# Performance work log

Measured on AMD Instinct MI355X. Metric: run time of the kernel, lower is better.

The kernel has to match this reference:

```python
import jax, jax.numpy as jnp
import numpy as np

P = 3  # spline degree in both u and v (init_kwargs degrees=[3,3])


def _knot_vector(n_cp, p):
    # clamped uniform knot vector, length n_cp+p+1 (matches calculate_knot_vectors)
    kv = np.concatenate([np.zeros(p), np.linspace(0.0, 1.0, n_cp - p + 1), np.ones(p)])
    return jnp.asarray(kv.astype(np.float32))


def _basis_and_deriv(u, spans, knots, p):
    # Cox-de Boor basis functions and 1st derivatives (NURBS Book A2.3), vectorized
    # u, spans: [S,F,E]; knots: 1D. Returns (N, dN) each [S,F,E,p+1].
    left = [None] * (p + 1)
    right = [None] * (p + 1)
    ndu = [[None] * (p + 1) for _ in range(p + 1)]
    ndu[0][0] = jnp.ones_like(u)
    for j in range(1, p + 1):
        left[j] = u - knots[spans - j + 1]
        right[j] = knots[spans + j] - u
        saved = jnp.zeros_like(u)
        for r in range(j):
            ndu[j][r] = right[r + 1] + left[j - r]  # knot differences
            tmp = ndu[r][j - 1] / ndu[j][r]
            ndu[r][j] = saved + right[r + 1] * tmp
            saved = left[j - r] * tmp
        ndu[j][j] = saved
    n = 1  # nth_derivative = 1
    ders = [[jnp.zeros_like(u) for _ in range(p + 1)] for _ in range(n + 1)]
    for j in range(p + 1):
        ders[0][j] = ndu[j][p]
    for r in range(p + 1):
        a = [[jnp.zeros_like(u) for _ in range(p + 1)] for _ in range(2)]
        a[0][0] = jnp.ones_like(u)
        s1, s2 = 0, 1
        for k in range(1, n + 1):
            d = jnp.zeros_like(u)
            rk, pk = r - k, p - k
            if r >= k:
                a[s2][0] = a[s1][0] / ndu[pk + 1][rk]
                d = a[s2][0] * ndu[rk][pk]
            j1 = 1 if rk >= -1 else -rk
            j2 = k - 1 if r - 1 <= pk else p - r
            for jj in range(j1, j2 + 1):
                a[s2][jj] = (a[s1][jj] - a[s1][jj - 1]) / ndu[pk + 1][rk + jj]
                d = d + a[s2][jj] * ndu[rk + jj][pk]
            if r <= pk:
                a[s2][k] = -a[s1][k - 1] / ndu[pk + 1][r]
                d = d + a[s2][k] * ndu[r][pk]
            ders[k][r] = d
            s1, s2 = s2, s1
    # multiply by p!/(p-k)! factor for k=1
    N0 = jnp.stack(ders[0], axis=-1)
    N1 = jnp.stack([ders[1][j] * p for j in range(p + 1)], axis=-1)
    return N0, N1


def _forward(evaluation_points, control_points):
    S, F, n_u, n_v, _ = control_points.shape
    p = P
    knots_u = _knot_vector(n_u, p)
    knots_v = _knot_vector(n_v, p)
    u = evaluation_points[..., 0]
    v = evaluation_points[..., 1]
    # uniform knot span search: floor(t * n_intervals) + degree (find_spans, uniform branch)
    spans_u = jnp.clip(jnp.floor(u * (n_u - p)).astype(jnp.int32) + p, p, n_u - 1)
    spans_v = jnp.clip(jnp.floor(v * (n_v - p)).astype(jnp.int32) + p, p, n_v - 1)
    bu0, bu1 = _basis_and_deriv(u, spans_u, knots_u, p)  # [S,F,E,p+1]
    bv0, bv1 = _basis_and_deriv(v, spans_v, knots_v, p)
    offs = jnp.arange(p + 1)
    iu = spans_u[..., None] - p + offs  # [S,F,E,p+1] control indices in u
    iv = spans_v[..., None] - p + offs
    sidx = jnp.arange(S)[:, None, None, None, None]
    fidx = jnp.arange(F)[None, :, None, None, None]
    # gather local (p+1)x(p+1) control net per eval point: [S,F,E,p+1,p+1,3]
    g = control_points[sidx, fidx, iu[..., :, None], iv[..., None, :]]
    pts = jnp.einsum('sfeijc,sfei,sfej->sfec', g, bu0, bv0)
    du = jnp.einsum('sfeijc,sfei,sfej->sfec', g, bu1, bv0)
    dv = jnp.einsum('sfeijc,sfei,sfej->sfec', g, bu0, bv1)
    nrm = jnp.cross(du, dv)
    nrm = nrm / (jnp.linalg.norm(nrm, axis=-1, keepdims=True) + 1e-12)
    ones = jnp.ones_like(pts[..., :1])
    points4 = jnp.concatenate([pts, ones], axis=-1)
    normals4 = jnp.concatenate([nrm, jnp.zeros_like(ones)], axis=-1)
    return points4, normals4


def setup_inputs() -> dict:
    key = jax.random.key(0)
    k1, k2 = jax.random.split(key)
    S, F, E = 4, 4, 65536
    N_CP = 32
    evaluation_points = jax.random.uniform(k1, (S, F, E, 2), dtype=jnp.float32)
    control_points = jax.random.normal(k2, (S, F, N_CP, N_CP, 3), dtype=jnp.float32)
    return {"evaluation_points": evaluation_points, "control_points": control_points}


def reference(evaluation_points, control_points):
    return _forward(evaluation_points, control_points)
```

## Files before the change

### kernel.cpp

```cpp
#include <hip/hip_runtime.h>

typedef __fp16 half2_t __attribute__((ext_vector_type(2)));

#define S_DIM 4
#define F_DIM 4
#define E_DIM 65536
#define NCP   32

union H2U { unsigned u; half2_t h; };

__device__ __forceinline__ unsigned pkh(float a, float b) {
    H2U c; c.h = __builtin_amdgcn_cvt_pkrtz(a, b);
    return c.u;
}
__device__ __forceinline__ half2_t ash2(unsigned u) {
    H2U c; c.u = u;
    return c.h;
}

__device__ __forceinline__ void basis3(float u, float fs, float* N0, float* N1) {
    const float h = 1.0f / 29.0f;
    const float b = fs * h;
    const float L1 = u - b;
    const float L2 = u - fmaxf(b - h, 0.0f);
    const float L3 = u - fmaxf(b - 2.0f * h, 0.0f);
    const float R1 = (b + h) - u;
    const float R2 = fminf(b + 2.0f * h, 1.0f) - u;
    const float R3 = fminf(b + 3.0f * h, 1.0f) - u;
    const float i10 = __builtin_amdgcn_rcpf(R1 + L1);
    const float v01 = R1 * i10;
    const float v11 = L1 * i10;
    const float i20 = __builtin_amdgcn_rcpf(R1 + L2);
    float t = v01 * i20;
    const float v02 = R1 * t;
    float s = L2 * t;
    const float i21 = __builtin_amdgcn_rcpf(R2 + L1);
    t = v11 * i21;
    const float v12 = s + R2 * t;
    const float v22 = L1 * t;
    const float i30 = __builtin_amdgcn_rcpf(R1 + L3);
    t = v02 * i30;
    N0[0] = R1 * t;
    s = L3 * t;
    const float i31 = __builtin_amdgcn_rcpf(R2 + L2);
    t = v12 * i31;
    N0[1] = s + R2 * t;
    s = L2 * t;
    const float i32 = __builtin_amdgcn_rcpf(R3 + L1);
    t = v22 * i32;
    N0[2] = s + R3 * t;
    N0[3] = L1 * t;
    const float a0 = v02 * i30, a1 = v12 * i31, a2 = v22 * i32;
    N1[0] = -3.0f * a0;
    N1[1] = 3.0f * (a0 - a1);
    N1[2] = 3.0f * (a1 - a2);
    N1[3] = 3.0f * a2;
}

__global__ __launch_bounds__(256) void nurbs_eval_kernel(
    const float* __restrict__ ep,
    const float* __restrict__ cp,
    float* __restrict__ out)
{
    __shared__ unsigned sm[3 * 32 * 33];

    const int sf  = blockIdx.y;
    const int tid = threadIdx.x;

    {
        const int u = tid >> 3, m = tid & 7;
        const float* rowp = cp + ((size_t)sf * 1024 + (size_t)u * 32) * 3;
        const int o = 12 * m;
        const float4 Ld0 = *(const float4*)(rowp + o);
        const float4 Ld1 = *(const float4*)(rowp + o + 4);
        const float4 Ld2 = *(const float4*)(rowp + o + 8);
        const float4 Ld3 = *(const float4*)(rowp + ((m == 7) ? 80 : (o + 12)));
        float f[16];
        f[0]=Ld0.x; f[1]=Ld0.y; f[2]=Ld0.z; f[3]=Ld0.w;
        f[4]=Ld1.x; f[5]=Ld1.y; f[6]=Ld1.z; f[7]=Ld1.w;
        f[8]=Ld2.x; f[9]=Ld2.y; f[10]=Ld2.z; f[11]=Ld2.w;
        f[12]=Ld3.x; f[13]=Ld3.y; f[14]=Ld3.z; f[15]=Ld3.w;
        unsigned* E0 = sm;
        unsigned* E1 = sm + 1056;
        unsigned* E2 = sm + 2112;
#pragma unroll
        for (int e = 0; e < 4; ++e) {
            const int v = 4 * m + e;
            const int a = u * 33 + v;
            E0[a] = pkh(f[3*e+0], f[3*e+3]);
            E1[a] = pkh(f[3*e+1], f[3*e+4]);
            E2[a] = pkh(f[3*e+2], f[3*e+5]);
        }
    }
    __syncthreads();

    const int e   = blockIdx.x * 256 + tid;
    const int idx = sf * E_DIM + e;

    const float2 uvp = ((const float2*)ep)[idx];
    const float uu = uvp.x, vv = uvp.y;

    const float fsu = fminf(fmaxf(floorf(uu * 29.0f), 0.0f), 28.0f);
    const float fsv = fminf(fmaxf(floorf(vv * 29.0f), 0.0f), 28.0f);
    const int bu = (int)fsu, bv = (int)fsv;

    float bu0[4], bu1[4], bv0[4], bv1[4];
    basis3(uu, fsu, bu0, bu1);
    basis3(vv, fsv, bv0, bv1);

    const half2_t w00 = __builtin_amdgcn_cvt_pkrtz(bv0[0], bv0[1]);
    const half2_t w01 = __builtin_amdgcn_cvt_pkrtz(bv0[2], bv0[3]);
    const half2_t w10 = __builtin_amdgcn_cvt_pkrtz(bv1[0], bv1[1]);
    const half2_t w11 = __builtin_amdgcn_cvt_pkrtz(bv1[2], bv1[3]);

    const unsigned* E0 = sm;
    const unsigned* E1 = sm + 1056;
    const unsigned* E2 = sm + 2112;
    const int base = 33 * bu + bv;

    float px=0.f, py=0.f, pz=0.f;
    float dux=0.f, duy=0.f, duz=0.f;
    float dvx=0.f, dvy=0.f, dvz=0.f;

#pragma unroll
    for (int i = 0; i < 4; ++i) {
        const int a = base + 33 * i;
        const half2_t x0 = ash2(E0[a]), x1 = ash2(E0[a + 2]);
        const half2_t y0 = ash2(E1[a]), y1 = ash2(E1[a + 2]);
        const half2_t z0 = ash2(E2[a]), z1 = ash2(E2[a + 2]);
        const float t0x = __builtin_amdgcn_fdot2(x1, w01, __builtin_amdgcn_fdot2(x0, w00, 0.0f, false), false);
        const float t1x = __builtin_amdgcn_fdot2(x1, w11, __builtin_amdgcn_fdot2(x0, w10, 0.0f, false), false);
        const float t0y = __builtin_amdgcn_fdot2(y1, w01, __builtin_amdgcn_fdot2(y0, w00, 0.0f, false), false);
        const float t1y = __builtin_amdgcn_fdot2(y1, w11, __builtin_amdgcn_fdot2(y0, w10, 0.0f, false), false);
        const float t0z = __builtin_amdgcn_fdot2(z1, w01, __builtin_amdgcn_fdot2(z0, w00, 0.0f, false), false);
        const float t1z = __builtin_amdgcn_fdot2(z1, w11, __builtin_amdgcn_fdot2(z0, w10, 0.0f, false), false);
        px  = fmaf(bu0[i], t0x, px);  py  = fmaf(bu0[i], t0y, py);  pz  = fmaf(bu0[i], t0z, pz);
        dux = fmaf(bu1[i], t0x, dux); duy = fmaf(bu1[i], t0y, duy); duz = fmaf(bu1[i], t0z, duz);
        dvx = fmaf(bu0[i], t1x, dvx); dvy = fmaf(bu0[i], t1y, dvy); dvz = fmaf(bu0[i], t1z, dvz);
    }

    float nx = duy * dvz - duz * dvy;
    float ny = duz * dvx - dux * dvz;
    float nz = dux * dvy - duy * dvx;
    float n2 = nx * nx + ny * ny + nz * nz;
    const float du2 = dux*dux + duy*duy + duz*duz;
    const float dv2 = dvx*dvx + dvy*dvy + dvz*dvz;

    if (n2 < 2e-3f * (du2 * dv2)) {
        const float* patch = cp + (size_t)sf * 3072;
        float DUX=0.f, DUY=0.f, DUZ=0.f, DVX=0.f, DVY=0.f, DVZ=0.f;
#pragma unroll
        for (int i = 0; i < 4; ++i) {
            float s0x=0.f, s0y=0.f, s0z=0.f, s1x=0.f, s1y=0.f, s1z=0.f;
#pragma unroll
            for (int j = 0; j < 4; ++j) {
                const float* p = patch + (((bu + i) * 32) + (bv + j)) * 3;
                const float gx = p[0], gy = p[1], gz = p[2];
                s0x = fmaf(gx, bv0[j], s0x); s0y = fmaf(gy, bv0[j], s0y); s0z = fmaf(gz, bv0[j], s0z);
                s1x = fmaf(gx, bv1[j], s1x); s1y = fmaf(gy, bv1[j], s1y); s1z = fmaf(gz, bv1[j], s1z);
            }
            DUX = fmaf(bu1[i], s0x, DUX); DUY = fmaf(bu1[i], s0y, DUY); DUZ = fmaf(bu1[i], s0z, DUZ);
            DVX = fmaf(bu0[i], s1x, DVX); DVY = fmaf(bu0[i], s1y, DVY); DVZ = fmaf(bu0[i], s1z, DVZ);
        }
        nx = DUY * DVZ - DUZ * DVY;
        ny = DUZ * DVX - DUX * DVZ;
        nz = DUX * DVY - DUY * DVX;
        n2 = nx * nx + ny * ny + nz * nz;
    }

    const float inv = __builtin_amdgcn_rcpf(sqrtf(n2) + 1e-12f);
    nx *= inv; ny *= inv; nz *= inv;

    float4* outv = (float4*)out;
    outv[idx] = make_float4(px, py, pz, 1.0f);
    outv[(size_t)S_DIM * F_DIM * E_DIM + idx] = make_float4(nx, ny, nz, 0.0f);
}

extern "C" void kernel_launch(void* const* d_in, const int* in_sizes, int n_in,
                              void* d_out, int out_size, void* d_ws, size_t ws_size,
                              hipStream_t stream) {
    const float* ep = (const float*)d_in[0];
    const float* cp = (const float*)d_in[1];
    float* out = (float*)d_out;

    dim3 grid(E_DIM / 256, S_DIM * F_DIM);
    dim3 block(256);
    hipLaunchKernelGGL(nurbs_eval_kernel, grid, block, 0, stream, ep, cp, out);
}
```

Before: 19.35 us.

## Process four points per thread and overlap control-net staging with basis computation

Each block now handles four evaluation points per thread, cutting the block count and the per-block cost of staging the control net into shared memory. The evaluation-point loads and basis computations for all four points are issued before the shared-memory fill and barrier, so global latency overlaps that work. The fp32 fallback threshold for ill-conditioned normals is raised from 2e-3 to 6e-3, which sends more points through the exact path, and launch bounds now request 4 blocks per CU. Keeping four points' basis values live raises register pressure, and the grid shrinks to 1024 blocks, which may leave the GPU underoccupied.

```diff
diff --git a/kernel.cpp b/kernel.cpp
--- a/kernel.cpp
+++ b/kernel.cpp
@@ -6,6 +6,7 @@
 #define F_DIM 4
 #define E_DIM 65536
 #define NCP   32
+#define PPT   4
 
 union H2U { unsigned u; half2_t h; };
 
@@ -57,7 +58,7 @@
     N1[3] = 3.0f * a2;
 }
 
-__global__ __launch_bounds__(256) void nurbs_eval_kernel(
+__global__ __launch_bounds__(256, 4) void nurbs_eval_kernel(
     const float* __restrict__ ep,
     const float* __restrict__ cp,
     float* __restrict__ out)
@@ -67,14 +68,39 @@
     const int sf  = blockIdx.y;
     const int tid = threadIdx.x;
 
+    const int su_ = tid >> 3, sm_ = tid & 7;
+    const float* rowp = cp + ((size_t)sf * 1024 + (size_t)su_ * 32) * 3;
+    const int o = 12 * sm_;
+    const float4 Ld0 = *(const float4*)(rowp + o);
+    const float4 Ld1 = *(const float4*)(rowp + o + 4);
+    const float4 Ld2 = *(const float4*)(rowp + o + 8);
+    const float4 Ld3 = *(const float4*)(rowp + ((sm_ == 7) ? 80 : (o + 12)));
+
+    const int e0  = blockIdx.x * (256 * PPT) + tid;
+    const int idx0 = sf * E_DIM + e0;
+
+    float2  UV[PPT];
+    float   BU0[PPT][4], BU1[PPT][4];
+    unsigned W[PPT][4];
+    int     BASE[PPT];
+
+#pragma unroll
+    for (int k = 0; k < PPT; ++k) {
+        UV[k] = ((const float2*)ep)[idx0 + k * 256];
+        const float uu = UV[k].x, vv = UV[k].y;
+        const float fsu = fminf(fmaxf(floorf(uu * 29.0f), 0.0f), 28.0f);
+        const float fsv = fminf(fmaxf(floorf(vv * 29.0f), 0.0f), 28.0f);
+        float bv0[4], bv1[4];
+        basis3(uu, fsu, BU0[k], BU1[k]);
+        basis3(vv, fsv, bv0, bv1);
+        W[k][0] = pkh(bv0[0], bv0[1]);
+        W[k][1] = pkh(bv0[2], bv0[3]);
+        W[k][2] = pkh(bv1[0], bv1[1]);
+        W[k][3] = pkh(bv1[2], bv1[3]);
+        BASE[k] = 33 * (int)fsu + (int)fsv;
+    }
+
     {
-        const int u = tid >> 3, m = tid & 7;
-        const float* rowp = cp + ((size_t)sf * 1024 + (size_t)u * 32) * 3;
-        const int o = 12 * m;
-        const float4 Ld0 = *(const float4*)(rowp + o);
-        const float4 Ld1 = *(const float4*)(rowp + o + 4);
-        const float4 Ld2 = *(const float4*)(rowp + o + 8);
-        const float4 Ld3 = *(const float4*)(rowp + ((m == 7) ? 80 : (o + 12)));
         float f[16];
         f[0]=Ld0.x; f[1]=Ld0.y; f[2]=Ld0.z; f[3]=Ld0.w;
         f[4]=Ld1.x; f[5]=Ld1.y; f[6]=Ld1.z; f[7]=Ld1.w;
@@ -85,8 +111,8 @@
         unsigned* E2 = sm + 2112;
 #pragma unroll
         for (int e = 0; e < 4; ++e) {
-            const int v = 4 * m + e;
-            const int a = u * 33 + v;
+            const int v = 4 * sm_ + e;
+            const int a = su_ * 33 + v;
             E0[a] = pkh(f[3*e+0], f[3*e+3]);
             E1[a] = pkh(f[3*e+1], f[3*e+4]);
             E2[a] = pkh(f[3*e+2], f[3*e+5]);
@@ -94,86 +120,83 @@
     }
     __syncthreads();
 
-    const int e   = blockIdx.x * 256 + tid;
-    const int idx = sf * E_DIM + e;
-
-    const float2 uvp = ((const float2*)ep)[idx];
-    const float uu = uvp.x, vv = uvp.y;
-
-    const float fsu = fminf(fmaxf(floorf(uu * 29.0f), 0.0f), 28.0f);
-    const float fsv = fminf(fmaxf(floorf(vv * 29.0f), 0.0f), 28.0f);
-    const int bu = (int)fsu, bv = (int)fsv;
-
-    float bu0[4], bu1[4], bv0[4], bv1[4];
-    basis3(uu, fsu, bu0, bu1);
-    basis3(vv, fsv, bv0, bv1);
-
-    const half2_t w00 = __builtin_amdgcn_cvt_pkrtz(bv0[0], bv0[1]);
-    const half2_t w01 = __builtin_amdgcn_cvt_pkrtz(bv0[2], bv0[3]);
-    const half2_t w10 = __builtin_amdgcn_cvt_pkrtz(bv1[0], bv1[1]);
-    const half2_t w11 = __builtin_amdgcn_cvt_pkrtz(bv1[2], bv1[3]);
-
     const unsigned* E0 = sm;
     const unsigned* E1 = sm + 1056;
     const unsigned* E2 = sm + 2112;
-    const int base = 33 * bu + bv;
-
-    float px=0.f, py=0.f, pz=0.f;
-    float dux=0.f, duy=0.f, duz=0.f;
-    float dvx=0.f, dvy=0.f, dvz=0.f;
-
-#pragma unroll
-    for (int i = 0; i < 4; ++i) {
-        const int a = base + 33 * i;
-        const half2_t x0 = ash2(E0[a]), x1 = ash2(E0[a + 2]);
-        const half2_t y0 = ash2(E1[a]), y1 = ash2(E1[a + 2]);
-        const half2_t z0 = ash2(E2[a]), z1 = ash2(E2[a + 2]);
-        const float t0x = __builtin_amdgcn_fdot2(x1, w01, __builtin_amdgcn_fdot2(x0, w00, 0.0f, false), false);
-        const float t1x = __builtin_amdgcn_fdot2(x1, w11, __builtin_amdgcn_fdot2(x0, w10, 0.0f, false), false);
-        const float t0y = __builtin_amdgcn_fdot2(y1, w01, __builtin_amdgcn_fdot2(y0, w00, 0.0f, false), false);
-        const float t1y = __builtin_amdgcn_fdot2(y1, w11, __builtin_amdgcn_fdot2(y0, w10, 0.0f, false), false);
-        const float t0z = __builtin_amdgcn_fdot2(z1, w01, __builtin_amdgcn_fdot2(z0, w00, 0.0f, false), false);
-        const float t1z = __builtin_amdgcn_fdot2(z1, w11, __builtin_amdgcn_fdot2(z0, w10, 0.0f, false), false);
-        px  = fmaf(bu0[i], t0x, px);  py  = fmaf(bu0[i], t0y, py);  pz  = fmaf(bu0[i], t0z, pz);
-        dux = fmaf(bu1[i], t0x, dux); duy = fmaf(bu1[i], t0y, duy); duz = fmaf(bu1[i], t0z, duz);
-        dvx = fmaf(bu0[i], t1x, dvx); dvy = fmaf(bu0[i], t1y, dvy); dvz = fmaf(bu0[i], t1z, dvz);
+    float4* outv = (float4*)out;
+
+#pragma unroll
+    for (int k = 0; k < PPT; ++k) {
+        const int base = BASE[k];
+        const half2_t w00 = ash2(W[k][0]);
+        const half2_t w01 = ash2(W[k][1]);
+        const half2_t w10 = ash2(W[k][2]);
+        const half2_t w11 = ash2(W[k][3]);
+
+        float px=0.f, py=0.f, pz=0.f;
+        float dux=0.f, duy=0.f, duz=0.f;
+        float dvx=0.f, dvy=0.f, dvz=0.f;
+
+#pragma unroll
+        for (int i = 0; i < 4; ++i) {
+            const int a = base + 33 * i;
+            const half2_t x0 = ash2(E0[a]), x1 = ash2(E0[a + 2]);
+            const half2_t y0 = ash2(E1[a]), y1 = ash2(E1[a + 2]);
+            const half2_t z0 = ash2(E2[a]), z1 = ash2(E2[a + 2]);
+            const float t0x = __builtin_amdgcn_fdot2(x1, w01, __builtin_amdgcn_fdot2(x0, w00, 0.0f, false), false);
+            const float t1x = __builtin_amdgcn_fdot2(x1, w11, __builtin_amdgcn_fdot2(x0, w10, 0.0f, false), false);
+            const float t0y = __builtin_amdgcn_fdot2(y1, w01, __builtin_amdgcn_fdot2(y0, w00, 0.0f, false), false);
+            const float t1y = __builtin_amdgcn_fdot2(y1, w11, __builtin_amdgcn_fdot2(y0, w10, 0.0f, false), false);
+            const float t0z = __builtin_amdgcn_fdot2(z1, w01, __builtin_amdgcn_fdot2(z0, w00, 0.0f, false), false);
+            const float t1z = __builtin_amdgcn_fdot2(z1, w11, __builtin_amdgcn_fdot2(z0, w10, 0.0f, false), false);
+            px  = fmaf(BU0[k][i], t0x, px);  py  = fmaf(BU0[k][i], t0y, py);  pz  = fmaf(BU0[k][i], t0z, pz);
+            dux = fmaf(BU1[k][i], t0x, dux); duy = fmaf(BU1[k][i], t0y, duy); duz = fmaf(BU1[k][i], t0z, duz);
+            dvx = fmaf(BU0[k][i], t1x, dvx); dvy = fmaf(BU0[k][i], t1y, dvy); dvz = fmaf(BU0[k][i], t1z, dvz);
+        }
+
+        float nx = duy * dvz - duz * dvy;
+        float ny = duz * dvx - dux * dvz;
+        float nz = dux * dvy - duy * dvx;
+        float n2 = nx * nx + ny * ny + nz * nz;
+        const float du2 = dux*dux + duy*duy + duz*duz;
+        const float dv2 = dvx*dvx + dvy*dvy + dvz*dvz;
+
+        if (n2 < 6e-3f * (du2 * dv2)) {
+            const float uu = UV[k].x, vv = UV[k].y;
+            const float fsu = fminf(fmaxf(floorf(uu * 29.0f), 0.0f), 28.0f);
+            const float fsv = fminf(fmaxf(floorf(vv * 29.0f), 0.0f), 28.0f);
+            const int bu = (int)fsu, bv = (int)fsv;
+            float fu0[4], fu1[4], fv0[4], fv1[4];
+            basis3(uu, fsu, fu0, fu1);
+            basis3(vv, fsv, fv0, fv1);
+            const float* patch = cp + (size_t)sf * 3072;
+            float DUX=0.f, DUY=0.f, DUZ=0.f, DVX=0.f, DVY=0.f, DVZ=0.f;
+#pragma unroll
+            for (int i = 0; i < 4; ++i) {
+                float s0x=0.f, s0y=0.f, s0z=0.f, s1x=0.f, s1y=0.f, s1z=0.f;
+#pragma unroll
+                for (int j = 0; j < 4; ++j) {
+                    const float* p = patch + (((bu + i) * 32) + (bv + j)) * 3;
+                    const float gx = p[0], gy = p[1], gz = p[2];
+                    s0x = fmaf(gx, fv0[j], s0x); s0y = fmaf(gy, fv0[j], s0y); s0z = fmaf(gz, fv0[j], s0z);
+                    s1x = fmaf(gx, fv1[j], s1x); s1y = fmaf(gy, fv1[j], s1y); s1z = fmaf(gz, fv1[j], s1z);
+                }
+                DUX = fmaf(fu1[i], s0x, DUX); DUY = fmaf(fu1[i], s0y, DUY); DUZ = fmaf(fu1[i], s0z, DUZ);
+                DVX = fmaf(fu0[i], s1x, DVX); DVY = fmaf(fu0[i], s1y, DVY); DVZ = fmaf(fu0[i], s1z, DVZ);
+            }
+            nx = DUY * DVZ - DUZ * DVY;
+            ny = DUZ * DVX - DUX * DVZ;
+            nz = DUX * DVY - DUY * DVX;
+            n2 = nx * nx + ny * ny + nz * nz;
+        }
+
+        const float inv = __builtin_amdgcn_rcpf(sqrtf(n2) + 1e-12f);
+        nx *= inv; ny *= inv; nz *= inv;
+
+        const int idx = idx0 + k * 256;
+        outv[idx] = make_float4(px, py, pz, 1.0f);
+        outv[(size_t)S_DIM * F_DIM * E_DIM + idx] = make_float4(nx, ny, nz, 0.0f);
     }
-
-    float nx = duy * dvz - duz * dvy;
-    float ny = duz * dvx - dux * dvz;
-    float nz = dux * dvy - duy * dvx;
-    float n2 = nx * nx + ny * ny + nz * nz;
-    const float du2 = dux*dux + duy*duy + duz*duz;
-    const float dv2 = dvx*dvx + dvy*dvy + dvz*dvz;
-
-    if (n2 < 2e-3f * (du2 * dv2)) {
-        const float* patch = cp + (size_t)sf * 3072;
-        float DUX=0.f, DUY=0.f, DUZ=0.f, DVX=0.f, DVY=0.f, DVZ=0.f;
-#pragma unroll
-        for (int i = 0; i < 4; ++i) {
-            float s0x=0.f, s0y=0.f, s0z=0.f, s1x=0.f, s1y=0.f, s1z=0.f;
-#pragma unroll
-            for (int j = 0; j < 4; ++j) {
-                const float* p = patch + (((bu + i) * 32) + (bv + j)) * 3;
-                const float gx = p[0], gy = p[1], gz = p[2];
-                s0x = fmaf(gx, bv0[j], s0x); s0y = fmaf(gy, bv0[j], s0y); s0z = fmaf(gz, bv0[j], s0z);
-                s1x = fmaf(gx, bv1[j], s1x); s1y = fmaf(gy, bv1[j], s1y); s1z = fmaf(gz, bv1[j], s1z);
-            }
-            DUX = fmaf(bu1[i], s0x, DUX); DUY = fmaf(bu1[i], s0y, DUY); DUZ = fmaf(bu1[i], s0z, DUZ);
-            DVX = fmaf(bu0[i], s1x, DVX); DVY = fmaf(bu0[i], s1y, DVY); DVZ = fmaf(bu0[i], s1z, DVZ);
-        }
-        nx = DUY * DVZ - DUZ * DVY;
-        ny = DUZ * DVX - DUX * DVZ;
-        nz = DUX * DVY - DUY * DVX;
-        n2 = nx * nx + ny * ny + nz * nz;
-    }
-
-    const float inv = __builtin_amdgcn_rcpf(sqrtf(n2) + 1e-12f);
-    nx *= inv; ny *= inv; nz *= inv;
-
-    float4* outv = (float4*)out;
-    outv[idx] = make_float4(px, py, pz, 1.0f);
-    outv[(size_t)S_DIM * F_DIM * E_DIM + idx] = make_float4(nx, ny, nz, 0.0f);
 }
 
 extern "C" void kernel_launch(void* const* d_in, const int* in_sizes, int n_in,
@@ -183,7 +206,7 @@
     const float* cp = (const float*)d_in[1];
     float* out = (float*)d_out;
 
-    dim3 grid(E_DIM / 256, S_DIM * F_DIM);
+    dim3 grid(E_DIM / (256 * PPT), S_DIM * F_DIM);
     dim3 block(256);
     hipLaunchKernelGGL(nurbs_eval_kernel, grid, block, 0, stream, ep, cp, out);
 }
```

After: 34.51 us. +78.3%, slower.
